# Kernel tuning notes

Measured on AMD Instinct MI355X. Metric: run time of the kernel, lower is better.

Reference implementation:

```python
import jax, jax.numpy as jnp
import numpy as np

N_QUBITS = 10
N_LAYERS = 4
DIM = 2 ** N_QUBITS  # 1024
IN_FEATURES = 512
OUT_FEATURES = 64
BATCH = 4096


def setup_inputs() -> dict:
    key = jax.random.key(0)
    ks = jax.random.split(key, 6)
    return {
        "x": jax.random.normal(ks[0], (BATCH, IN_FEATURES), dtype=jnp.float32),
        "W_pre": jax.random.normal(ks[1], (DIM, IN_FEATURES), dtype=jnp.float32) / np.float32(np.sqrt(IN_FEATURES)),
        "b_pre": jnp.zeros((DIM,), dtype=jnp.float32),
        "q_weights": jax.random.normal(ks[2], (N_LAYERS, N_QUBITS, 3), dtype=jnp.float32),
        "W_post": jax.random.normal(ks[3], (OUT_FEATURES, N_QUBITS), dtype=jnp.float32) / np.float32(np.sqrt(N_QUBITS)),
        "b_post": jnp.zeros((OUT_FEATURES,), dtype=jnp.float32),
    }


def _rot_matrices(w):
    # w: [L, n, 3] -> PennyLane Rot(phi, theta, omega) = RZ(omega) RY(theta) RZ(phi)
    phi, theta, omega = w[..., 0], w[..., 1], w[..., 2]
    c = jnp.cos(theta / 2).astype(jnp.complex64)
    s = jnp.sin(theta / 2).astype(jnp.complex64)
    e_mm = jnp.exp(-0.5j * (phi + omega))
    e_pp = jnp.exp(0.5j * (phi + omega))
    e_pm = jnp.exp(0.5j * (phi - omega))
    e_mp = jnp.exp(-0.5j * (phi - omega))
    row0 = jnp.stack([e_mm * c, -e_pm * s], axis=-1)
    row1 = jnp.stack([e_mp * s, e_pp * c], axis=-1)
    return jnp.stack([row0, row1], axis=-2)  # [L, n, 2, 2] complex64


def _apply_1q(psi, U, wire):
    # psi: [B, 2, 2, ..., 2]; apply 2x2 unitary U on qubit `wire` (axis wire+1)
    axis = wire + 1
    psi = jnp.moveaxis(psi, axis, -1)
    psi = psi @ U.T  # new[a] = sum_b U[a,b] psi[b]
    return jnp.moveaxis(psi, -1, axis)


def _cnot(psi, control, target):
    ca, ta = control + 1, target + 1
    p0 = jax.lax.index_in_dim(psi, 0, ca, keepdims=True)
    p1 = jax.lax.index_in_dim(psi, 1, ca, keepdims=True)
    p1 = jnp.flip(p1, axis=ta)  # flip target amplitudes where control = 1
    return jnp.concatenate([p0, p1], axis=ca)


def _quantum_forward(amps, q_weights):
    # AmplitudeEmbedding(normalize=True) + StronglyEntanglingLayers + PauliZ expvals, batched.
    B = amps.shape[0]
    norm = jnp.sqrt(jnp.sum(amps * amps, axis=1, keepdims=True))
    psi = (amps / norm).astype(jnp.complex64).reshape((B,) + (2,) * N_QUBITS)
    U = _rot_matrices(q_weights)
    for l in range(N_LAYERS):
        for w in range(N_QUBITS):
            psi = _apply_1q(psi, U[l, w], w)
        r = (l % (N_QUBITS - 1)) + 1  # PennyLane default ranges
        for w in range(N_QUBITS):
            psi = _cnot(psi, w, (w + r) % N_QUBITS)
    probs = psi.real ** 2 + psi.imag ** 2
    axes_all = tuple(range(1, N_QUBITS + 1))
    z = []
    for i in range(N_QUBITS):
        other = tuple(a for a in axes_all if a != i + 1)
        marg = jnp.sum(probs, axis=other)  # [B, 2]
        z.append(marg[:, 0] - marg[:, 1])
    return jnp.stack(z, axis=1)  # [B, n_qubits]


def reference(x, W_pre, b_pre, q_weights, W_post, b_post):
    h = jax.nn.relu(x @ W_pre.T + b_pre)          # [B, 2^n]
    z = _quantum_forward(h, q_weights)            # [B, n_qubits]
    return z @ W_post.T + b_post                  # [B, out_features]
```

## Files before the change

### kernel.cpp

```cpp
#include <hip/hip_runtime.h>
#include <hip/hip_bf16.h>
#include <math.h>

#define NQ   10
#define DIM  1024
#define NL   4
#define INF  512
#define OUTF 64
#define MBATCH 4096

typedef _Float16 half8 __attribute__((ext_vector_type(8)));
typedef float f32x4 __attribute__((ext_vector_type(4)));
typedef float f32x2 __attribute__((ext_vector_type(2)));

#define WS_H16  0
#define WS_X16  (8u * 1024u * 1024u)
#define WS_W16  (12u * 1024u * 1024u)
#define WS_SU   (13u * 1024u * 1024u)

constexpr int fstep(int j, int r) {
    for (int w2 = NQ - 1; w2 >= 0; --w2) {
        const int cb = 9 - w2;
        const int tb = 9 - ((w2 + r) % NQ);
        j ^= ((j >> cb) & 1) << tb;
    }
    return j;
}
constexpr int ifstep(int j, int r) {
    for (int w2 = 0; w2 < NQ; ++w2) {
        const int cb = 9 - w2;
        const int tb = 9 - ((w2 + r) % NQ);
        j ^= ((j >> cb) & 1) << tb;
    }
    return j;
}
constexpr int sigma_fwd(int l, int x) {
    for (int t = l - 1; t >= 0; --t) x = fstep(x, t + 1);
    return x;
}
constexpr int sigma_inv(int l, int s) {
    for (int t = 0; t < l; ++t) s = ifstep(s, t + 1);
    return s;
}
constexpr int gate_m(int l, int b) { return sigma_fwd(l, 1 << b); }
constexpr int gate_g(int l, int b) {
    int g = 0;
    for (int j = 0; j < NQ; ++j)
        if ((sigma_inv(l, 1 << j) >> b) & 1) g |= 1 << j;
    return g;
}
struct QM { int v[NQ]; };
constexpr QM make_qm() {
    QM q{};
    for (int w = 0; w < NQ; ++w) {
        const int B = 9 - w;
        int m = 0;
        for (int j = 0; j < NQ; ++j)
            if ((sigma_inv(NL, 1 << j) >> B) & 1) m |= 1 << j;
        q.v[w] = m;
    }
    return q;
}
constexpr QM QMASKS = make_qm();

__global__ __launch_bounds__(256) void setup_kernel(
    const float* __restrict__ x, const float* __restrict__ w,
    const float* __restrict__ qw, _Float16* __restrict__ x16,
    _Float16* __restrict__ w16, float* __restrict__ su)
{
    const int bid = blockIdx.x;
    const int tid = threadIdx.x;
    if (bid < 1024) {
        const int base = bid * 2048 + tid * 8;
        float4 a = *reinterpret_cast<const float4*>(x + base);
        float4 b = *reinterpret_cast<const float4*>(x + base + 4);
        half8 o = {(_Float16)a.x, (_Float16)a.y, (_Float16)a.z, (_Float16)a.w,
                   (_Float16)b.x, (_Float16)b.y, (_Float16)b.z, (_Float16)b.w};
        *reinterpret_cast<half8*>(x16 + base) = o;
    } else if (bid < 1280) {
        const int base = (bid - 1024) * 2048 + tid * 8;
        float4 a = *reinterpret_cast<const float4*>(w + base);
        float4 b = *reinterpret_cast<const float4*>(w + base + 4);
        half8 o = {(_Float16)a.x, (_Float16)a.y, (_Float16)a.z, (_Float16)a.w,
                   (_Float16)b.x, (_Float16)b.y, (_Float16)b.z, (_Float16)b.w};
        *reinterpret_cast<half8*>(w16 + base) = o;
    } else {
        if (tid < NL * NQ) {
            float phi = qw[tid * 3 + 0], theta = qw[tid * 3 + 1], omega = qw[tid * 3 + 2];
            float st, ct; sincosf(0.5f * theta, &st, &ct);
            float spm, cpm; sincosf(0.5f * (phi - omega), &spm, &cpm);
            float spp, cpp; sincosf(0.5f * (phi + omega), &spp, &cpp);
            float* o = su + tid * 8;
            o[0] =  cpp * ct; o[1] = -spp * ct;
            o[2] = -cpm * st; o[3] = -spm * st;
            o[4] =  cpm * st; o[5] = -spm * st;
            o[6] =  cpp * ct; o[7] =  spp * ct;
        }
    }
}

__global__ __launch_bounds__(256) void gemm16_kernel(
    const _Float16* __restrict__ X, const _Float16* __restrict__ W,
    const float* __restrict__ bias, _Float16* __restrict__ H)
{
    constexpr int BM = 128, BN = 64, BK = 32, LDP = BK + 8;
    __shared__ _Float16 As[BM][LDP];
    __shared__ _Float16 Bs[BN][LDP];

    const int tid = threadIdx.x;
    const int wave = tid >> 6, lane = tid & 63;
    const int wm = wave >> 1, wn = wave & 1;
    const int l15 = lane & 15, lk = (lane >> 4) * 8;

    const int arow = tid >> 1, ahalf = tid & 1;
    const int brow = tid & 63, bseg = tid >> 6;

    const _Float16* ag = X + (size_t)(blockIdx.x * BM + arow) * INF + ahalf * 16;
    const _Float16* bg = W + (size_t)(blockIdx.y * BN + brow) * INF + bseg * 8;

    f32x4 acc[4][2] = {};

    for (int k0 = 0; k0 < INF; k0 += BK) {
        half8 av0 = *reinterpret_cast<const half8*>(ag + k0);
        half8 av1 = *reinterpret_cast<const half8*>(ag + k0 + 8);
        half8 bv  = *reinterpret_cast<const half8*>(bg + k0);
        __syncthreads();
        *reinterpret_cast<half8*>(&As[arow][ahalf * 16])     = av0;
        *reinterpret_cast<half8*>(&As[arow][ahalf * 16 + 8]) = av1;
        *reinterpret_cast<half8*>(&Bs[brow][bseg * 8])       = bv;
        __syncthreads();
        half8 bfr0 = *reinterpret_cast<const half8*>(&Bs[wn * 32 + l15][lk]);
        half8 bfr1 = *reinterpret_cast<const half8*>(&Bs[wn * 32 + 16 + l15][lk]);
#pragma unroll
        for (int mi = 0; mi < 4; ++mi) {
            half8 afr = *reinterpret_cast<const half8*>(&As[wm * 64 + mi * 16 + l15][lk]);
            acc[mi][0] = __builtin_amdgcn_mfma_f32_16x16x32_f16(afr, bfr0, acc[mi][0], 0, 0, 0);
            acc[mi][1] = __builtin_amdgcn_mfma_f32_16x16x32_f16(afr, bfr1, acc[mi][1], 0, 0, 0);
        }
    }

    const int crow0 = blockIdx.x * BM + wm * 64;
    const int ccol0 = blockIdx.y * BN + wn * 32;
#pragma unroll
    for (int ni = 0; ni < 2; ++ni) {
        const int col = ccol0 + ni * 16 + l15;
        const float bb = bias[col];
#pragma unroll
        for (int mi = 0; mi < 4; ++mi) {
#pragma unroll
            for (int r = 0; r < 4; ++r) {
                const int row = crow0 + mi * 16 + (lane >> 4) * 4 + r;
                const float o = fmaxf(acc[mi][ni][r] + bb, 0.f);
                H[(size_t)row * DIM + col] = (_Float16)o;
            }
        }
    }
}

template<int MHI>
__device__ __forceinline__ float lx(float v, int lane) {
    if constexpr (MHI == 0)
        return v;
    else if constexpr (MHI == 1)
        return __int_as_float(__builtin_amdgcn_mov_dpp(__float_as_int(v), 0xB1, 0xF, 0xF, false));
    else if constexpr (MHI == 2)
        return __int_as_float(__builtin_amdgcn_mov_dpp(__float_as_int(v), 0x4E, 0xF, 0xF, false));
    else if constexpr (MHI == 3)
        return __int_as_float(__builtin_amdgcn_mov_dpp(__float_as_int(v), 0x1B, 0xF, 0xF, false));
    else if constexpr (MHI == 8)
        return __int_as_float(__builtin_amdgcn_mov_dpp(__float_as_int(v), 0x128, 0xF, 0xF, false));
    else if constexpr (MHI < 32)
        return __int_as_float(__builtin_amdgcn_ds_swizzle(__float_as_int(v), 0x1F | (MHI << 10)));
    else
        return __int_as_float(__builtin_amdgcn_ds_bpermute((lane ^ MHI) << 2, __float_as_int(v)));
}

template<int L, int W>
__device__ __forceinline__ void apply_gate(f32x2 rr[8], f32x2 ii[8],
                                           const float* __restrict__ su, int lane)
{
    constexpr int b   = 9 - W;
    constexpr int m   = gate_m(L, b);
    constexpr int g   = gate_g(L, b);
    constexpr int MHI = m >> 4, MLO = m & 15;
    constexpr int GHI = g >> 4, GLO = g & 15;

    const float4 ua = *reinterpret_cast<const float4*>(su + (L * NQ + W) * 8);
    const float4 ub = *reinterpret_cast<const float4*>(su + (L * NQ + W) * 8 + 4);
    const bool hl = __builtin_popcount(lane & GHI) & 1;

    const float cmr0 = hl ? ub.z : ua.x, cmi0 = hl ? ub.w : ua.y;
    const float cpr0 = hl ? ub.x : ua.z, cpi0 = hl ? ub.y : ua.w;
    const float cmr1 = hl ? ua.x : ub.z, cmi1 = hl ? ua.y : ub.w;
    const float cpr1 = hl ? ua.z : ub.x, cpi1 = hl ? ua.w : ub.y;

    float pr[16], pi[16];
#pragma unroll
    for (int k = 0; k < 16; ++k) {
        const int kp = k ^ MLO;
        const float vr = (kp & 1) ? rr[kp >> 1].y : rr[kp >> 1].x;
        const float vi = (kp & 1) ? ii[kp >> 1].y : ii[kp >> 1].x;
        pr[k] = lx<MHI>(vr, lane);
        pi[k] = lx<MHI>(vi, lane);
    }
#pragma unroll
    for (int j = 0; j < 8; ++j) {
        const int k0 = 2 * j, k1 = 2 * j + 1;
        const int h0 = __builtin_popcount(k0 & GLO) & 1;
        const int h1 = __builtin_popcount(k1 & GLO) & 1;
        f32x2 CMR, CMI, CPR, CPI, PR, PI;
        CMR.x = h0 ? cmr1 : cmr0;  CMR.y = h1 ? cmr1 : cmr0;
        CMI.x = h0 ? cmi1 : cmi0;  CMI.y = h1 ? cmi1 : cmi0;
        CPR.x = h0 ? cpr1 : cpr0;  CPR.y = h1 ? cpr1 : cpr0;
        CPI.x = h0 ? cpi1 : cpi0;  CPI.y = h1 ? cpi1 : cpi0;
        PR.x = pr[k0]; PR.y = pr[k1];
        PI.x = pi[k0]; PI.y = pi[k1];
        const f32x2 R = rr[j], I = ii[j];
        rr[j] = R * CMR - I * CMI + PR * CPR - PI * CPI;
        ii[j] = I * CMR + R * CMI + PI * CPR + PR * CPI;
    }
}

template<int L>
__device__ __forceinline__ void apply_layer(f32x2 rr[8], f32x2 ii[8],
                                            const float* __restrict__ su, int lane)
{
    apply_gate<L, 0>(rr, ii, su, lane);
    apply_gate<L, 1>(rr, ii, su, lane);
    apply_gate<L, 2>(rr, ii, su, lane);
    apply_gate<L, 3>(rr, ii, su, lane);
    apply_gate<L, 4>(rr, ii, su, lane);
    apply_gate<L, 5>(rr, ii, su, lane);
    apply_gate<L, 6>(rr, ii, su, lane);
    apply_gate<L, 7>(rr, ii, su, lane);
    apply_gate<L, 8>(rr, ii, su, lane);
    apply_gate<L, 9>(rr, ii, su, lane);
}

__global__ __launch_bounds__(256) void quantum_kernel(
    const _Float16* __restrict__ Hbuf, const float* __restrict__ sug,
    const float* __restrict__ W_post, const float* __restrict__ b_post,
    float* __restrict__ out)
{
    const int lane = threadIdx.x;
    const int row  = blockIdx.x * 4 + threadIdx.y;

    const _Float16* hr = Hbuf + (size_t)row * DIM + (lane << 4);
    f32x2 rr[8], ii[8];
    {
        half8 h0 = *reinterpret_cast<const half8*>(hr);
        half8 h1 = *reinterpret_cast<const half8*>(hr + 8);
#pragma unroll
        for (int j = 0; j < 4; ++j) {
            rr[j].x     = (float)h0[2 * j];     rr[j].y     = (float)h0[2 * j + 1];
            rr[j + 4].x = (float)h1[2 * j];     rr[j + 4].y = (float)h1[2 * j + 1];
            ii[j]     = f32x2{0.f, 0.f};
            ii[j + 4] = f32x2{0.f, 0.f};
        }
    }
    f32x2 n2 = f32x2{0.f, 0.f};
#pragma unroll
    for (int j = 0; j < 8; ++j) n2 += rr[j] * rr[j];
    float nrm = n2.x + n2.y;
#pragma unroll
    for (int m2 = 1; m2 < 64; m2 <<= 1) nrm += __shfl_xor(nrm, m2, 64);
    const float inv_nrm = 1.0f / nrm;

    apply_layer<0>(rr, ii, sug, lane);
    apply_layer<1>(rr, ii, sug, lane);
    apply_layer<2>(rr, ii, sug, lane);
    apply_layer<3>(rr, ii, sug, lane);

    f32x2 P[8];
#pragma unroll
    for (int j = 0; j < 8; ++j) P[j] = rr[j] * rr[j] + ii[j] * ii[j];

    float z[NQ];
#pragma unroll
    for (int w = 0; w < NQ; ++w) {
        const int q = QMASKS.v[w];
        const int qhi = q >> 4, qlo = q & 15;
        float zl = 0.f;
#pragma unroll
        for (int j = 0; j < 8; ++j) {
            const float s0 = (__builtin_popcount((2 * j) & qlo) & 1) ? -1.f : 1.f;
            const float s1 = (__builtin_popcount((2 * j + 1) & qlo) & 1) ? -1.f : 1.f;
            zl += s0 * P[j].x;
            zl += s1 * P[j].y;
        }
        if (__builtin_popcount(lane & qhi) & 1) zl = -zl;
#pragma unroll
        for (int m2 = 1; m2 < 64; m2 <<= 1) zl += __shfl_xor(zl, m2, 64);
        z[w] = zl * inv_nrm;
    }

    float o = b_post[lane];
#pragma unroll
    for (int w = 0; w < NQ; ++w)
        o = fmaf(z[w], W_post[lane * NQ + w], o);
    out[(size_t)row * OUTF + lane] = o;
}

extern "C" void kernel_launch(void* const* d_in, const int* in_sizes, int n_in,
                              void* d_out, int out_size, void* d_ws, size_t ws_size,
                              hipStream_t stream) {
    const float* x      = (const float*)d_in[0];
    const float* W_pre  = (const float*)d_in[1];
    const float* b_pre  = (const float*)d_in[2];
    const float* qw     = (const float*)d_in[3];
    const float* W_post = (const float*)d_in[4];
    const float* b_post = (const float*)d_in[5];
    float* out = (float*)d_out;

    char* ws = (char*)d_ws;
    _Float16* h16 = (_Float16*)(ws + WS_H16);
    _Float16* x16 = (_Float16*)(ws + WS_X16);
    _Float16* w16 = (_Float16*)(ws + WS_W16);
    float*    su  = (float*)   (ws + WS_SU);

    setup_kernel<<<1281, 256, 0, stream>>>(x, W_pre, qw, x16, w16, su);
    dim3 g1(MBATCH / 128, DIM / 64);
    gemm16_kernel<<<g1, 256, 0, stream>>>(x16, w16, b_pre, h16);
    quantum_kernel<<<MBATCH / 4, dim3(64, 4), 0, stream>>>(h16, su, W_post, b_post, out);
}
```

Before: 62.26 us.

## Process two batch rows per wavefront and use permlane/DPP cross-lane exchanges

Each wavefront now simulates two state vectors, interleaving the gate applications so their cross-lane exchanges and FMAs can overlap, and halves the grid. Lane exchanges gain more DPP patterns (row_mirror, row_half_mirror) and permlane16/32 swaps where the builtins exist, replacing ds_swizzle/bpermute traffic through LDS. The all-reductions use the same DPP/permlane path in place of __shfl_xor. The cost is roughly doubled register pressure per thread, which may lower occupancy or cause spills, and a grid with half as many blocks.

```diff
diff --git a/kernel.cpp b/kernel.cpp
--- a/kernel.cpp
+++ b/kernel.cpp
@@ -17,6 +17,12 @@
 #define WS_X16  (8u * 1024u * 1024u)
 #define WS_W16  (12u * 1024u * 1024u)
 #define WS_SU   (13u * 1024u * 1024u)
+
+#if __has_builtin(__builtin_amdgcn_permlane16_swap) && __has_builtin(__builtin_amdgcn_permlane32_swap)
+#define HAVE_PL 1
+#else
+#define HAVE_PL 0
+#endif
 
 constexpr int fstep(int j, int r) {
     for (int w2 = NQ - 1; w2 >= 0; --w2) {
@@ -157,22 +163,51 @@
     }
 }
 
+constexpr bool dpp_ok(int m) {
+    return m == 0 || m == 1 || m == 2 || m == 3 || m == 7 || m == 8 || m == 15;
+}
+constexpr int dpp_ctrl(int m) {
+    return m == 1 ? 0xB1 : m == 2 ? 0x4E : m == 3 ? 0x1B :
+           m == 7 ? 0x141 : m == 8 ? 0x128 : 0x140;
+}
+
 template<int MHI>
-__device__ __forceinline__ float lx(float v, int lane) {
+__device__ __forceinline__ int lxi(int v, int lane) {
     if constexpr (MHI == 0)
         return v;
-    else if constexpr (MHI == 1)
-        return __int_as_float(__builtin_amdgcn_mov_dpp(__float_as_int(v), 0xB1, 0xF, 0xF, false));
-    else if constexpr (MHI == 2)
-        return __int_as_float(__builtin_amdgcn_mov_dpp(__float_as_int(v), 0x4E, 0xF, 0xF, false));
-    else if constexpr (MHI == 3)
-        return __int_as_float(__builtin_amdgcn_mov_dpp(__float_as_int(v), 0x1B, 0xF, 0xF, false));
-    else if constexpr (MHI == 8)
-        return __int_as_float(__builtin_amdgcn_mov_dpp(__float_as_int(v), 0x128, 0xF, 0xF, false));
+    else if constexpr (dpp_ok(MHI))
+        return __builtin_amdgcn_mov_dpp(v, dpp_ctrl(MHI), 0xF, 0xF, false);
+#if HAVE_PL
+    else if constexpr ((MHI & 32) && dpp_ok(MHI & 15)) {
+        auto q = __builtin_amdgcn_permlane32_swap(v, v, false, false);
+        const int r = (lane & 32) ? q[0] : q[1];
+        return lxi<MHI & 31>(r, lane);
+    }
+    else if constexpr ((MHI & 16) && dpp_ok(MHI & 15)) {
+        auto q = __builtin_amdgcn_permlane16_swap(v, v, false, false);
+        const int r = (lane & 16) ? q[0] : q[1];
+        return lxi<MHI & 15>(r, lane);
+    }
+#endif
     else if constexpr (MHI < 32)
-        return __int_as_float(__builtin_amdgcn_ds_swizzle(__float_as_int(v), 0x1F | (MHI << 10)));
+        return __builtin_amdgcn_ds_swizzle(v, 0x1F | (MHI << 10));
     else
-        return __int_as_float(__builtin_amdgcn_ds_bpermute((lane ^ MHI) << 2, __float_as_int(v)));
+        return __builtin_amdgcn_ds_bpermute((lane ^ MHI) << 2, v);
+}
+
+template<int MHI>
+__device__ __forceinline__ float lxf(float v, int lane) {
+    return __int_as_float(lxi<MHI>(__float_as_int(v), lane));
+}
+
+__device__ __forceinline__ float allred(float v, int lane) {
+    v += lxf<1>(v, lane);
+    v += lxf<2>(v, lane);
+    v += lxf<4>(v, lane);
+    v += lxf<8>(v, lane);
+    v += lxf<16>(v, lane);
+    v += lxf<32>(v, lane);
+    return v;
 }
 
 template<int L, int W>
@@ -200,8 +235,8 @@
         const int kp = k ^ MLO;
         const float vr = (kp & 1) ? rr[kp >> 1].y : rr[kp >> 1].x;
         const float vi = (kp & 1) ? ii[kp >> 1].y : ii[kp >> 1].x;
-        pr[k] = lx<MHI>(vr, lane);
-        pi[k] = lx<MHI>(vi, lane);
+        pr[k] = lxf<MHI>(vr, lane);
+        pi[k] = lxf<MHI>(vi, lane);
     }
 #pragma unroll
     for (int j = 0; j < 8; ++j) {
@@ -222,60 +257,47 @@
 }
 
 template<int L>
-__device__ __forceinline__ void apply_layer(f32x2 rr[8], f32x2 ii[8],
-                                            const float* __restrict__ su, int lane)
-{
-    apply_gate<L, 0>(rr, ii, su, lane);
-    apply_gate<L, 1>(rr, ii, su, lane);
-    apply_gate<L, 2>(rr, ii, su, lane);
-    apply_gate<L, 3>(rr, ii, su, lane);
-    apply_gate<L, 4>(rr, ii, su, lane);
-    apply_gate<L, 5>(rr, ii, su, lane);
-    apply_gate<L, 6>(rr, ii, su, lane);
-    apply_gate<L, 7>(rr, ii, su, lane);
-    apply_gate<L, 8>(rr, ii, su, lane);
-    apply_gate<L, 9>(rr, ii, su, lane);
-}
-
-__global__ __launch_bounds__(256) void quantum_kernel(
-    const _Float16* __restrict__ Hbuf, const float* __restrict__ sug,
-    const float* __restrict__ W_post, const float* __restrict__ b_post,
-    float* __restrict__ out)
-{
-    const int lane = threadIdx.x;
-    const int row  = blockIdx.x * 4 + threadIdx.y;
-
-    const _Float16* hr = Hbuf + (size_t)row * DIM + (lane << 4);
-    f32x2 rr[8], ii[8];
-    {
-        half8 h0 = *reinterpret_cast<const half8*>(hr);
-        half8 h1 = *reinterpret_cast<const half8*>(hr + 8);
-#pragma unroll
-        for (int j = 0; j < 4; ++j) {
-            rr[j].x     = (float)h0[2 * j];     rr[j].y     = (float)h0[2 * j + 1];
-            rr[j + 4].x = (float)h1[2 * j];     rr[j + 4].y = (float)h1[2 * j + 1];
-            ii[j]     = f32x2{0.f, 0.f};
-            ii[j + 4] = f32x2{0.f, 0.f};
-        }
+__device__ __forceinline__ void apply_layer2(f32x2 rA[8], f32x2 iA[8],
+                                             f32x2 rB[8], f32x2 iB[8],
+                                             const float* __restrict__ su, int lane)
+{
+    apply_gate<L, 0>(rA, iA, su, lane); apply_gate<L, 0>(rB, iB, su, lane);
+    apply_gate<L, 1>(rA, iA, su, lane); apply_gate<L, 1>(rB, iB, su, lane);
+    apply_gate<L, 2>(rA, iA, su, lane); apply_gate<L, 2>(rB, iB, su, lane);
+    apply_gate<L, 3>(rA, iA, su, lane); apply_gate<L, 3>(rB, iB, su, lane);
+    apply_gate<L, 4>(rA, iA, su, lane); apply_gate<L, 4>(rB, iB, su, lane);
+    apply_gate<L, 5>(rA, iA, su, lane); apply_gate<L, 5>(rB, iB, su, lane);
+    apply_gate<L, 6>(rA, iA, su, lane); apply_gate<L, 6>(rB, iB, su, lane);
+    apply_gate<L, 7>(rA, iA, su, lane); apply_gate<L, 7>(rB, iB, su, lane);
+    apply_gate<L, 8>(rA, iA, su, lane); apply_gate<L, 8>(rB, iB, su, lane);
+    apply_gate<L, 9>(rA, iA, su, lane); apply_gate<L, 9>(rB, iB, su, lane);
+}
+
+__device__ __forceinline__ void load_row(const _Float16* __restrict__ hr,
+                                         f32x2 rr[8], f32x2 ii[8], float& nrm,
+                                         int lane)
+{
+    half8 h0 = *reinterpret_cast<const half8*>(hr);
+    half8 h1 = *reinterpret_cast<const half8*>(hr + 8);
+#pragma unroll
+    for (int j = 0; j < 4; ++j) {
+        rr[j].x     = (float)h0[2 * j]; rr[j].y     = (float)h0[2 * j + 1];
+        rr[j + 4].x = (float)h1[2 * j]; rr[j + 4].y = (float)h1[2 * j + 1];
+        ii[j]     = f32x2{0.f, 0.f};
+        ii[j + 4] = f32x2{0.f, 0.f};
     }
     f32x2 n2 = f32x2{0.f, 0.f};
 #pragma unroll
     for (int j = 0; j < 8; ++j) n2 += rr[j] * rr[j];
-    float nrm = n2.x + n2.y;
-#pragma unroll
-    for (int m2 = 1; m2 < 64; m2 <<= 1) nrm += __shfl_xor(nrm, m2, 64);
-    const float inv_nrm = 1.0f / nrm;
-
-    apply_layer<0>(rr, ii, sug, lane);
-    apply_layer<1>(rr, ii, sug, lane);
-    apply_layer<2>(rr, ii, sug, lane);
-    apply_layer<3>(rr, ii, sug, lane);
-
+    nrm = allred(n2.x + n2.y, lane);
+}
+
+__device__ __forceinline__ void expvals(const f32x2 rr[8], const f32x2 ii[8],
+                                        float inv_nrm, float z[NQ], int lane)
+{
     f32x2 P[8];
 #pragma unroll
     for (int j = 0; j < 8; ++j) P[j] = rr[j] * rr[j] + ii[j] * ii[j];
-
-    float z[NQ];
 #pragma unroll
     for (int w = 0; w < NQ; ++w) {
         const int q = QMASKS.v[w];
@@ -289,16 +311,47 @@
             zl += s1 * P[j].y;
         }
         if (__builtin_popcount(lane & qhi) & 1) zl = -zl;
-#pragma unroll
-        for (int m2 = 1; m2 < 64; m2 <<= 1) zl += __shfl_xor(zl, m2, 64);
-        z[w] = zl * inv_nrm;
-    }
-
-    float o = b_post[lane];
-#pragma unroll
-    for (int w = 0; w < NQ; ++w)
-        o = fmaf(z[w], W_post[lane * NQ + w], o);
-    out[(size_t)row * OUTF + lane] = o;
+        z[w] = allred(zl, lane) * inv_nrm;
+    }
+}
+
+__global__ __launch_bounds__(256) void quantum_kernel(
+    const _Float16* __restrict__ Hbuf, const float* __restrict__ sug,
+    const float* __restrict__ W_post, const float* __restrict__ b_post,
+    float* __restrict__ out)
+{
+    const int lane = threadIdx.x;
+    const int rowA = (blockIdx.x * 4 + threadIdx.y) * 2;
+    const int rowB = rowA + 1;
+
+    f32x2 rA[8], iA[8], rB[8], iB[8];
+    float nA, nB;
+    load_row(Hbuf + (size_t)rowA * DIM + (lane << 4), rA, iA, nA, lane);
+    load_row(Hbuf + (size_t)rowB * DIM + (lane << 4), rB, iB, nB, lane);
+    const float invA = 1.0f / nA;
+    const float invB = 1.0f / nB;
+
+    apply_layer2<0>(rA, iA, rB, iB, sug, lane);
+    apply_layer2<1>(rA, iA, rB, iB, sug, lane);
+    apply_layer2<2>(rA, iA, rB, iB, sug, lane);
+    apply_layer2<3>(rA, iA, rB, iB, sug, lane);
+
+    float zA[NQ], zB[NQ];
+    expvals(rA, iA, invA, zA, lane);
+    expvals(rB, iB, invB, zB, lane);
+
+    float wv[NQ];
+#pragma unroll
+    for (int w = 0; w < NQ; ++w) wv[w] = W_post[lane * NQ + w];
+    const float bb = b_post[lane];
+    float oA = bb, oB = bb;
+#pragma unroll
+    for (int w = 0; w < NQ; ++w) {
+        oA = fmaf(zA[w], wv[w], oA);
+        oB = fmaf(zB[w], wv[w], oB);
+    }
+    out[(size_t)rowA * OUTF + lane] = oA;
+    out[(size_t)rowB * OUTF + lane] = oB;
 }
 
 extern "C" void kernel_launch(void* const* d_in, const int* in_sizes, int n_in,
@@ -321,5 +374,5 @@
     setup_kernel<<<1281, 256, 0, stream>>>(x, W_pre, qw, x16, w16, su);
     dim3 g1(MBATCH / 128, DIM / 64);
     gemm16_kernel<<<g1, 256, 0, stream>>>(x16, w16, b_pre, h16);
-    quantum_kernel<<<MBATCH / 4, dim3(64, 4), 0, stream>>>(h16, su, W_post, b_post, out);
-}
+    quantum_kernel<<<MBATCH / 8, dim3(64, 4), 0, stream>>>(h16, su, W_post, b_post, out);
+}
```

Result: slower. 156.8 us (+151.9%).

## Split each quantum state across two waves with LDS exchange for one qubit

Applied to the files above, without the earlier changes.

The quantum kernel now runs each batch row on two wavefronts instead of one. Each lane holds 8 amplitudes instead of 16, and the qubit bit used least often by the gate masks is chosen at compile time to be the wave index. Gates that pair amplitudes across that bit exchange them through shared memory with block barriers. Reductions are combined through shared memory. The aim is to halve per-thread register state and raise occupancy, at the cost of extra syncthreads and LDS traffic on some gates and more blocks to launch.

```diff
diff --git a/kernel.cpp b/kernel.cpp
--- a/kernel.cpp
+++ b/kernel.cpp
@@ -62,6 +62,30 @@
     return q;
 }
 constexpr QM QMASKS = make_qm();
+
+constexpr int mask_at(int t) { return gate_m(t / 10, 9 - (t % 10)); }
+constexpr int pick_wbit() {
+    int best = 9, bc = 1000;
+    for (int j = 3; j <= 9; ++j) {
+        int c = 0;
+        for (int t = 0; t < 40; ++t) c += (mask_at(t) >> j) & 1;
+        if (c < bc) { bc = c; best = j; }
+    }
+    return best;
+}
+constexpr int WBIT = pick_wbit();
+struct LP { int v[6]; };
+constexpr LP make_lpos() {
+    LP p{}; int n = 0;
+    for (int j = 3; j <= 9; ++j) if (j != WBIT) p.v[n++] = j;
+    return p;
+}
+constexpr LP LPOS = make_lpos();
+constexpr int lx_extract(int m) {
+    int r = 0;
+    for (int t = 0; t < 6; ++t) if ((m >> LPOS.v[t]) & 1) r |= 1 << t;
+    return r;
+}
 
 __global__ __launch_bounds__(256) void setup_kernel(
     const float* __restrict__ x, const float* __restrict__ w,
@@ -158,56 +182,100 @@
 }
 
 template<int MHI>
-__device__ __forceinline__ float lx(float v, int lane) {
+__device__ __forceinline__ int lxi(int v, int lane) {
     if constexpr (MHI == 0)
         return v;
     else if constexpr (MHI == 1)
-        return __int_as_float(__builtin_amdgcn_mov_dpp(__float_as_int(v), 0xB1, 0xF, 0xF, false));
+        return __builtin_amdgcn_mov_dpp(v, 0xB1, 0xF, 0xF, false);
     else if constexpr (MHI == 2)
-        return __int_as_float(__builtin_amdgcn_mov_dpp(__float_as_int(v), 0x4E, 0xF, 0xF, false));
+        return __builtin_amdgcn_mov_dpp(v, 0x4E, 0xF, 0xF, false);
     else if constexpr (MHI == 3)
-        return __int_as_float(__builtin_amdgcn_mov_dpp(__float_as_int(v), 0x1B, 0xF, 0xF, false));
+        return __builtin_amdgcn_mov_dpp(v, 0x1B, 0xF, 0xF, false);
     else if constexpr (MHI == 8)
-        return __int_as_float(__builtin_amdgcn_mov_dpp(__float_as_int(v), 0x128, 0xF, 0xF, false));
+        return __builtin_amdgcn_mov_dpp(v, 0x128, 0xF, 0xF, false);
     else if constexpr (MHI < 32)
-        return __int_as_float(__builtin_amdgcn_ds_swizzle(__float_as_int(v), 0x1F | (MHI << 10)));
+        return __builtin_amdgcn_ds_swizzle(v, 0x1F | (MHI << 10));
     else
-        return __int_as_float(__builtin_amdgcn_ds_bpermute((lane ^ MHI) << 2, __float_as_int(v)));
+        return __builtin_amdgcn_ds_bpermute((lane ^ MHI) << 2, v);
+}
+
+template<int MHI>
+__device__ __forceinline__ float lxf(float v, int lane) {
+    return __int_as_float(lxi<MHI>(__float_as_int(v), lane));
+}
+
+__device__ __forceinline__ float allred(float v, int lane) {
+    v += lxf<1>(v, lane);
+    v += lxf<2>(v, lane);
+    v += lxf<4>(v, lane);
+    v += lxf<8>(v, lane);
+    v += lxf<16>(v, lane);
+    v += lxf<32>(v, lane);
+    return v;
 }
 
 template<int L, int W>
-__device__ __forceinline__ void apply_gate(f32x2 rr[8], f32x2 ii[8],
-                                           const float* __restrict__ su, int lane)
+__device__ __forceinline__ void apply_gate(f32x2 rr[4], f32x2 ii[4],
+                                           const float* __restrict__ su,
+                                           int lane, int wave,
+                                           f32x4 (*buf)[2][64])
 {
-    constexpr int b   = 9 - W;
-    constexpr int m   = gate_m(L, b);
-    constexpr int g   = gate_g(L, b);
-    constexpr int MHI = m >> 4, MLO = m & 15;
-    constexpr int GHI = g >> 4, GLO = g & 15;
+    constexpr int b = 9 - W;
+    constexpr int m = gate_m(L, b);
+    constexpr int g = gate_g(L, b);
+    constexpr int MW    = (m >> WBIT) & 1;
+    constexpr int MLANE = lx_extract(m);
+    constexpr int MREG  = m & 7;
+    constexpr int GW    = (g >> WBIT) & 1;
+    constexpr int GLANE = lx_extract(g);
+    constexpr int GREG  = g & 7;
 
     const float4 ua = *reinterpret_cast<const float4*>(su + (L * NQ + W) * 8);
     const float4 ub = *reinterpret_cast<const float4*>(su + (L * NQ + W) * 8 + 4);
-    const bool hl = __builtin_popcount(lane & GHI) & 1;
+    int hli = __builtin_popcount(lane & GLANE) & 1;
+    if constexpr (GW) hli ^= wave;
+    const bool hl = hli != 0;
 
     const float cmr0 = hl ? ub.z : ua.x, cmi0 = hl ? ub.w : ua.y;
     const float cpr0 = hl ? ub.x : ua.z, cpi0 = hl ? ub.y : ua.w;
     const float cmr1 = hl ? ua.x : ub.z, cmi1 = hl ? ua.y : ub.w;
     const float cpr1 = hl ? ua.z : ub.x, cpi1 = hl ? ua.w : ub.y;
 
-    float pr[16], pi[16];
-#pragma unroll
-    for (int k = 0; k < 16; ++k) {
-        const int kp = k ^ MLO;
-        const float vr = (kp & 1) ? rr[kp >> 1].y : rr[kp >> 1].x;
-        const float vi = (kp & 1) ? ii[kp >> 1].y : ii[kp >> 1].x;
-        pr[k] = lx<MHI>(vr, lane);
-        pi[k] = lx<MHI>(vi, lane);
-    }
-#pragma unroll
-    for (int j = 0; j < 8; ++j) {
+    float pr[8], pi[8];
+    if constexpr (MW == 0) {
+#pragma unroll
+        for (int k = 0; k < 8; ++k) {
+            const int kp = k ^ MREG;
+            const float vr = (kp & 1) ? rr[kp >> 1].y : rr[kp >> 1].x;
+            const float vi = (kp & 1) ? ii[kp >> 1].y : ii[kp >> 1].x;
+            pr[k] = lxf<MLANE>(vr, lane);
+            pi[k] = lxf<MLANE>(vi, lane);
+        }
+    } else {
+        buf[0][wave][lane] = f32x4{rr[0].x, rr[0].y, rr[1].x, rr[1].y};
+        buf[1][wave][lane] = f32x4{rr[2].x, rr[2].y, rr[3].x, rr[3].y};
+        buf[2][wave][lane] = f32x4{ii[0].x, ii[0].y, ii[1].x, ii[1].y};
+        buf[3][wave][lane] = f32x4{ii[2].x, ii[2].y, ii[3].x, ii[3].y};
+        __syncthreads();
+        const int pl = lane ^ MLANE;
+        const int pw = wave ^ 1;
+        const f32x4 R0 = buf[0][pw][pl];
+        const f32x4 R1 = buf[1][pw][pl];
+        const f32x4 I0 = buf[2][pw][pl];
+        const f32x4 I1 = buf[3][pw][pl];
+        __syncthreads();
+#pragma unroll
+        for (int k = 0; k < 8; ++k) {
+            const int kp = k ^ MREG;
+            pr[k] = (kp & 4) ? R1[kp & 3] : R0[kp & 3];
+            pi[k] = (kp & 4) ? I1[kp & 3] : I0[kp & 3];
+        }
+    }
+#pragma unroll
+    for (int j = 0; j < 4; ++j) {
         const int k0 = 2 * j, k1 = 2 * j + 1;
-        const int h0 = __builtin_popcount(k0 & GLO) & 1;
-        const int h1 = __builtin_popcount(k1 & GLO) & 1;
+        const int h0 = __builtin_popcount(k0 & GREG) & 1;
+        const int h1 = __builtin_popcount(k1 & GREG) & 1;
         f32x2 CMR, CMI, CPR, CPI, PR, PI;
         CMR.x = h0 ? cmr1 : cmr0;  CMR.y = h1 ? cmr1 : cmr0;
         CMI.x = h0 ? cmi1 : cmi0;  CMI.y = h1 ? cmi1 : cmi0;
@@ -222,83 +290,99 @@
 }
 
 template<int L>
-__device__ __forceinline__ void apply_layer(f32x2 rr[8], f32x2 ii[8],
-                                            const float* __restrict__ su, int lane)
+__device__ __forceinline__ void apply_layer(f32x2 rr[4], f32x2 ii[4],
+                                            const float* __restrict__ su,
+                                            int lane, int wave,
+                                            f32x4 (*buf)[2][64])
 {
-    apply_gate<L, 0>(rr, ii, su, lane);
-    apply_gate<L, 1>(rr, ii, su, lane);
-    apply_gate<L, 2>(rr, ii, su, lane);
-    apply_gate<L, 3>(rr, ii, su, lane);
-    apply_gate<L, 4>(rr, ii, su, lane);
-    apply_gate<L, 5>(rr, ii, su, lane);
-    apply_gate<L, 6>(rr, ii, su, lane);
-    apply_gate<L, 7>(rr, ii, su, lane);
-    apply_gate<L, 8>(rr, ii, su, lane);
-    apply_gate<L, 9>(rr, ii, su, lane);
-}
-
-__global__ __launch_bounds__(256) void quantum_kernel(
+    apply_gate<L, 0>(rr, ii, su, lane, wave, buf);
+    apply_gate<L, 1>(rr, ii, su, lane, wave, buf);
+    apply_gate<L, 2>(rr, ii, su, lane, wave, buf);
+    apply_gate<L, 3>(rr, ii, su, lane, wave, buf);
+    apply_gate<L, 4>(rr, ii, su, lane, wave, buf);
+    apply_gate<L, 5>(rr, ii, su, lane, wave, buf);
+    apply_gate<L, 6>(rr, ii, su, lane, wave, buf);
+    apply_gate<L, 7>(rr, ii, su, lane, wave, buf);
+    apply_gate<L, 8>(rr, ii, su, lane, wave, buf);
+    apply_gate<L, 9>(rr, ii, su, lane, wave, buf);
+}
+
+__global__ __launch_bounds__(128, 8) void quantum_kernel(
     const _Float16* __restrict__ Hbuf, const float* __restrict__ sug,
     const float* __restrict__ W_post, const float* __restrict__ b_post,
     float* __restrict__ out)
 {
+    __shared__ f32x4 buf[4][2][64];
+    __shared__ float sred[34];
+
     const int lane = threadIdx.x;
-    const int row  = blockIdx.x * 4 + threadIdx.y;
-
-    const _Float16* hr = Hbuf + (size_t)row * DIM + (lane << 4);
-    f32x2 rr[8], ii[8];
+    const int wave = threadIdx.y;
+    const int row  = blockIdx.x;
+
+    int pb = wave << WBIT;
+#pragma unroll
+    for (int t = 0; t < 6; ++t) pb |= ((lane >> t) & 1) << LPOS.v[t];
+
+    const _Float16* hr = Hbuf + (size_t)row * DIM + pb;
+    f32x2 rr[4], ii[4];
     {
         half8 h0 = *reinterpret_cast<const half8*>(hr);
-        half8 h1 = *reinterpret_cast<const half8*>(hr + 8);
 #pragma unroll
         for (int j = 0; j < 4; ++j) {
-            rr[j].x     = (float)h0[2 * j];     rr[j].y     = (float)h0[2 * j + 1];
-            rr[j + 4].x = (float)h1[2 * j];     rr[j + 4].y = (float)h1[2 * j + 1];
-            ii[j]     = f32x2{0.f, 0.f};
-            ii[j + 4] = f32x2{0.f, 0.f};
-        }
-    }
+            rr[j].x = (float)h0[2 * j]; rr[j].y = (float)h0[2 * j + 1];
+            ii[j] = f32x2{0.f, 0.f};
+        }
+    }
+
     f32x2 n2 = f32x2{0.f, 0.f};
 #pragma unroll
-    for (int j = 0; j < 8; ++j) n2 += rr[j] * rr[j];
-    float nrm = n2.x + n2.y;
-#pragma unroll
-    for (int m2 = 1; m2 < 64; m2 <<= 1) nrm += __shfl_xor(nrm, m2, 64);
-    const float inv_nrm = 1.0f / nrm;
-
-    apply_layer<0>(rr, ii, sug, lane);
-    apply_layer<1>(rr, ii, sug, lane);
-    apply_layer<2>(rr, ii, sug, lane);
-    apply_layer<3>(rr, ii, sug, lane);
-
-    f32x2 P[8];
-#pragma unroll
-    for (int j = 0; j < 8; ++j) P[j] = rr[j] * rr[j] + ii[j] * ii[j];
+    for (int j = 0; j < 4; ++j) n2 += rr[j] * rr[j];
+    float nw = allred(n2.x + n2.y, lane);
+    if (lane == 0) sred[32 + wave] = nw;
+    __syncthreads();
+    const float inv_nrm = 1.0f / (sred[32] + sred[33]);
+
+    apply_layer<0>(rr, ii, sug, lane, wave, buf);
+    apply_layer<1>(rr, ii, sug, lane, wave, buf);
+    apply_layer<2>(rr, ii, sug, lane, wave, buf);
+    apply_layer<3>(rr, ii, sug, lane, wave, buf);
+
+    f32x2 P[4];
+#pragma unroll
+    for (int j = 0; j < 4; ++j) P[j] = rr[j] * rr[j] + ii[j] * ii[j];
 
     float z[NQ];
 #pragma unroll
     for (int w = 0; w < NQ; ++w) {
         const int q = QMASKS.v[w];
-        const int qhi = q >> 4, qlo = q & 15;
+        const int qw_ = (q >> WBIT) & 1;
+        const int qlane = lx_extract(q);
+        const int qreg = q & 7;
         float zl = 0.f;
 #pragma unroll
-        for (int j = 0; j < 8; ++j) {
-            const float s0 = (__builtin_popcount((2 * j) & qlo) & 1) ? -1.f : 1.f;
-            const float s1 = (__builtin_popcount((2 * j + 1) & qlo) & 1) ? -1.f : 1.f;
-            zl += s0 * P[j].x;
-            zl += s1 * P[j].y;
-        }
-        if (__builtin_popcount(lane & qhi) & 1) zl = -zl;
-#pragma unroll
-        for (int m2 = 1; m2 < 64; m2 <<= 1) zl += __shfl_xor(zl, m2, 64);
-        z[w] = zl * inv_nrm;
-    }
-
-    float o = b_post[lane];
-#pragma unroll
-    for (int w = 0; w < NQ; ++w)
-        o = fmaf(z[w], W_post[lane * NQ + w], o);
-    out[(size_t)row * OUTF + lane] = o;
+        for (int j = 0; j < 4; ++j) {
+            const float s0 = (__builtin_popcount((2 * j) & qreg) & 1) ? -1.f : 1.f;
+            const float s1 = (__builtin_popcount((2 * j + 1) & qreg) & 1) ? -1.f : 1.f;
+            zl += s0 * P[j].x + s1 * P[j].y;
+        }
+        int neg = __builtin_popcount(lane & qlane) & 1;
+        neg ^= (wave & qw_);
+        if (neg) zl = -zl;
+        z[w] = allred(zl, lane);
+    }
+    if (lane == 0) {
+#pragma unroll
+        for (int w = 0; w < NQ; ++w) sred[wave * 16 + w] = z[w];
+    }
+    __syncthreads();
+
+    if (wave == 0) {
+        float o = b_post[lane];
+#pragma unroll
+        for (int w = 0; w < NQ; ++w)
+            o = fmaf((sred[w] + sred[16 + w]) * inv_nrm, W_post[lane * NQ + w], o);
+        out[(size_t)row * OUTF + lane] = o;
+    }
 }
 
 extern "C" void kernel_launch(void* const* d_in, const int* in_sizes, int n_in,
@@ -321,5 +405,5 @@
     setup_kernel<<<1281, 256, 0, stream>>>(x, W_pre, qw, x16, w16, su);
     dim3 g1(MBATCH / 128, DIM / 64);
     gemm16_kernel<<<g1, 256, 0, stream>>>(x16, w16, b_pre, h16);
-    quantum_kernel<<<MBATCH / 4, dim3(64, 4), 0, stream>>>(h16, su, W_post, b_post, out);
-}
+    quantum_kernel<<<MBATCH, dim3(64, 2), 0, stream>>>(h16, su, W_post, b_post, out);
+}
```

New measurement: 64.86 us. 1.04x slower.
